# Optimization experiments

Measured on AMD Instinct MI355X. Metric: run time of the kernel, lower is better.

Reference implementation:

```python
import jax, jax.numpy as jnp
import numpy as np

N, DIM, E = 50000, 128, 600000


def setup_inputs() -> dict:
    key = jax.random.key(0)
    ks = jax.random.split(key, 10)
    scale = 1.0 / np.sqrt(DIM)
    return {
        "s": jax.random.normal(ks[0], (N, DIM), jnp.float32),
        "v": jax.random.normal(ks[1], (N, 3, DIM), jnp.float32),
        "edge_index": jax.random.randint(ks[2], (2, E), 0, N, jnp.int32),
        # linear_q: Linear(dim, dim); stored as [in, out] so y = x @ W + b
        "Wq": jax.random.normal(ks[3], (DIM, DIM), jnp.float32) * scale,
        "bq": jnp.zeros((DIM,), jnp.float32),
        # linear_kv: Linear(dim, 3*dim)
        "Wkv": jax.random.normal(ks[4], (DIM, 3 * DIM), jnp.float32) * scale,
        "bkv": jnp.zeros((3 * DIM,), jnp.float32),
        # vec_mlp: Linear(dim, dim)
        "Wvec": jax.random.normal(ks[5], (DIM, DIM), jnp.float32) * scale,
        "bvec": jnp.zeros((DIM,), jnp.float32),
    }


def reference(s, v, edge_index, Wq, bq, Wkv, bkv, Wvec, bvec):
    n_nodes = s.shape[0]
    row, col = edge_index[0], edge_index[1]

    q = s @ Wq + bq                                   # [N, dim]
    kv = s @ Wkv + bkv                                # [N, 3*dim]
    k, v_s, v_v = jnp.split(kv, 3, axis=-1)           # each [N, dim]

    # edge attention weight: per-edge dot product of gathered q/k
    w = jnp.sum(q[row] * k[col], axis=-1, keepdims=True)   # [E, 1]

    edge_msg_s = w * v_s[col]                               # [E, dim]
    # [E,1,1] * [E,1,dim] * [E,3,dim] -> [E,3,dim]
    edge_msg_v = w[:, :, None] * v_v[col][:, None, :] * v[col]

    agg_s = jax.ops.segment_sum(edge_msg_s, row, num_segments=n_nodes)  # [N, dim]
    agg_v = jax.ops.segment_sum(edge_msg_v, row, num_segments=n_nodes)  # [N, 3, dim]

    s_out = s + agg_s
    v_out = v + (agg_v @ Wvec + bvec)
    return (s_out, v_out)
```

## Files before the change

### kernel.cpp

```cpp
#include <hip/hip_runtime.h>
#include <hip/hip_bf16.h>

typedef __attribute__((ext_vector_type(8))) __bf16 bf16x8;
typedef __attribute__((ext_vector_type(4))) float f32x4;


__global__ void hist_kernel(const int* __restrict__ row, int* __restrict__ cnt, int e) {
  int i = blockIdx.x * 256 + threadIdx.x;
  if (i < e) atomicAdd(&cnt[row[i]], 1);
}

__global__ __launch_bounds__(1024) void scan1_kernel(const int* __restrict__ cnt, int* __restrict__ off,
                                                     int* __restrict__ bsum, int n) {
  __shared__ int sh[1024];
  int tid = threadIdx.x;
  int i = blockIdx.x * 1024 + tid;
  int v = (i < n) ? cnt[i] : 0;
  sh[tid] = v;
  __syncthreads();
  for (int d = 1; d < 1024; d <<= 1) {
    int t = (tid >= d) ? sh[tid - d] : 0;
    __syncthreads();
    sh[tid] += t;
    __syncthreads();
  }
  if (i < n) off[i] = sh[tid] - v;
  if (tid == 1023) bsum[blockIdx.x] = sh[1023];
}

__global__ void scan2_kernel(int* bsum, int nb) {
  if (blockIdx.x == 0 && threadIdx.x == 0) {
    int run = 0;
    for (int b = 0; b < nb; b++) { int t = bsum[b]; bsum[b] = run; run += t; }
  }
}

__global__ __launch_bounds__(1024) void scan3_kernel(const int* __restrict__ bsum, int* __restrict__ off,
                                                     int* __restrict__ cursor, int n, int e) {
  int i = blockIdx.x * 1024 + threadIdx.x;
  if (i < n) { int o = off[i] + bsum[blockIdx.x]; off[i] = o; cursor[i] = o; }
  if (i == 0) off[n] = e;
}

__global__ void scatter_kernel(const int* __restrict__ row, const int* __restrict__ col,
                               int* __restrict__ cursor, int* __restrict__ scol, int e) {
  int i = blockIdx.x * 256 + threadIdx.x;
  if (i < e) { int r = row[i]; int pos = atomicAdd(&cursor[r], 1); scol[pos] = col[i]; }
}


__global__ void wprep_kernel(const float* __restrict__ Wq, const float* __restrict__ Wkv,
                             const float* __restrict__ Wvec, __bf16* __restrict__ Wt) {
  int idx = blockIdx.x * 256 + threadIdx.x;
  int c = idx >> 7, k = idx & 127;
  float w;
  if (c < 128)      w = Wq[k * 128 + c];
  else if (c < 512) w = Wkv[k * 384 + (c - 128)];
  else              w = Wvec[k * 128 + (c - 512)];
  Wt[idx] = (__bf16)w;
}


__global__ __launch_bounds__(256) void gemm1_mfma(
    const float* __restrict__ s, const __bf16* __restrict__ Wtg,
    const float* __restrict__ bq, const float* __restrict__ bkv,
    const float* __restrict__ v,
    __bf16* __restrict__ qb, __bf16* __restrict__ nodebuf, int n)
{
  __shared__ __bf16 sA[64 * 136];
  __shared__ char uB[34816];
  __bf16* sB = (__bf16*)uB;
  float*  sO = (float*)uB;

  const int tid = threadIdx.x;
  const int y = blockIdx.y;
  const int n0 = blockIdx.x * 64;
  const int drow = tid >> 2, dseg = tid & 3;
  const int dgn = n0 + drow;

  {
    float4 f[8];
    if (dgn < n) {
      #pragma unroll
      for (int i = 0; i < 8; i++)
        f[i] = *(const float4*)&s[(size_t)dgn * 128 + dseg * 32 + i * 4];
    } else {
      #pragma unroll
      for (int i = 0; i < 8; i++) f[i] = make_float4(0.f, 0.f, 0.f, 0.f);
    }
    #pragma unroll
    for (int i = 0; i < 4; i++) {
      bf16x8 pk;
      pk[0] = (__bf16)f[2*i].x;   pk[1] = (__bf16)f[2*i].y;
      pk[2] = (__bf16)f[2*i].z;   pk[3] = (__bf16)f[2*i].w;
      pk[4] = (__bf16)f[2*i+1].x; pk[5] = (__bf16)f[2*i+1].y;
      pk[6] = (__bf16)f[2*i+1].z; pk[7] = (__bf16)f[2*i+1].w;
      *(bf16x8*)&sA[drow * 136 + dseg * 32 + i * 8] = pk;
    }
  }
  {
    int row = tid >> 1, half = tid & 1;
    const __bf16* src = &Wtg[(size_t)(y * 128 + row) * 128 + half * 64];
    #pragma unroll
    for (int i = 0; i < 8; i++)
      *(bf16x8*)&sB[row * 136 + half * 64 + i * 8] = *(const bf16x8*)&src[i * 8];
  }
  __syncthreads();

  const int wave = tid >> 6, lane = tid & 63;
  const int lr = lane & 15, lg = lane >> 4;

  bf16x8 a[4];
  #pragma unroll
  for (int ks = 0; ks < 4; ks++)
    a[ks] = *(const bf16x8*)&sA[(wave * 16 + lr) * 136 + ks * 32 + lg * 8];

  f32x4 acc[8];
  #pragma unroll
  for (int cf = 0; cf < 8; cf++) {
    f32x4 c = {0.f, 0.f, 0.f, 0.f};
    #pragma unroll
    for (int ks = 0; ks < 4; ks++) {
      bf16x8 b = *(const bf16x8*)&sB[(cf * 16 + lr) * 136 + ks * 32 + lg * 8];
      c = __builtin_amdgcn_mfma_f32_16x16x32_bf16(a[ks], b, c, 0, 0, 0);
    }
    acc[cf] = c;
  }
  __syncthreads();

  #pragma unroll
  for (int cf = 0; cf < 8; cf++) {
    int cl = cf * 16 + lr;
    #pragma unroll
    for (int r = 0; r < 4; r++)
      sO[(wave * 16 + lg * 4 + r) * 132 + cl] = acc[cf][r];
  }
  __syncthreads();

  if (dgn < n) {
    if (y == 0) {
      #pragma unroll
      for (int i = 0; i < 4; i++) {
        int c0 = dseg * 32 + i * 8;
        bf16x8 pk;
        #pragma unroll
        for (int j = 0; j < 8; j++)
          pk[j] = (__bf16)(sO[drow * 132 + c0 + j] + bq[c0 + j]);
        *(bf16x8*)&qb[(size_t)dgn * 128 + c0] = pk;
      }
    } else if (y == 1 || y == 2) {
      const int boff = (y - 1) * 128;
      #pragma unroll
      for (int i = 0; i < 4; i++) {
        int c0 = dseg * 32 + i * 8;
        bf16x8 pk;
        #pragma unroll
        for (int j = 0; j < 8; j++)
          pk[j] = (__bf16)(sO[drow * 132 + c0 + j] + bkv[boff + c0 + j]);
        *(bf16x8*)&nodebuf[(size_t)dgn * 640 + boff + c0] = pk;
      }
    } else {
      float vv[32];
      #pragma unroll
      for (int j = 0; j < 32; j++)
        vv[j] = sO[drow * 132 + dseg * 32 + j] + bkv[256 + dseg * 32 + j];
      #pragma unroll
      for (int j3 = 0; j3 < 3; j3++) {
        #pragma unroll
        for (int i = 0; i < 4; i++) {
          int c0 = dseg * 32 + i * 8;
          float4 va = *(const float4*)&v[((size_t)dgn * 3 + j3) * 128 + c0];
          float4 vb = *(const float4*)&v[((size_t)dgn * 3 + j3) * 128 + c0 + 4];
          bf16x8 pk;
          pk[0] = (__bf16)(vv[i*8+0] * va.x); pk[1] = (__bf16)(vv[i*8+1] * va.y);
          pk[2] = (__bf16)(vv[i*8+2] * va.z); pk[3] = (__bf16)(vv[i*8+3] * va.w);
          pk[4] = (__bf16)(vv[i*8+4] * vb.x); pk[5] = (__bf16)(vv[i*8+5] * vb.y);
          pk[6] = (__bf16)(vv[i*8+6] * vb.z); pk[7] = (__bf16)(vv[i*8+7] * vb.w);
          *(bf16x8*)&nodebuf[(size_t)dgn * 640 + 256 + j3 * 128 + c0] = pk;
        }
      }
    }
  }
}


__device__ inline float2 bf2f(unsigned u) {
  float2 r;
  r.x = __uint_as_float((u & 0xffffu) << 16);
  r.y = __uint_as_float(u & 0xffff0000u);
  return r;
}

__device__ __forceinline__ float dpp_add(float x, const int ctrl) {
  int t;
  switch (ctrl) {
    case 0:  t = __builtin_amdgcn_update_dpp(0, __float_as_int(x), 0xB1, 0xF, 0xF, true); break;
    case 1:  t = __builtin_amdgcn_update_dpp(0, __float_as_int(x), 0x4E, 0xF, 0xF, true); break;
    case 2:  t = __builtin_amdgcn_update_dpp(0, __float_as_int(x), 0x141, 0xF, 0xF, true); break;
    default: t = __builtin_amdgcn_update_dpp(0, __float_as_int(x), 0x140, 0xF, 0xF, true); break;
  }
  return x + __int_as_float(t);
}

__device__ __forceinline__ float row16_sum(float x) {
  x = dpp_add(x, 0);
  x = dpp_add(x, 1);
  x = dpp_add(x, 2);
  x = dpp_add(x, 3);
  return x;
}

#define ACCP(arr, vec) do { float2 _t;                                                \
  _t = bf2f(vec.x); arr[0].x = fmaf(d, _t.x, arr[0].x); arr[0].y = fmaf(d, _t.y, arr[0].y); \
  _t = bf2f(vec.y); arr[1].x = fmaf(d, _t.x, arr[1].x); arr[1].y = fmaf(d, _t.y, arr[1].y); \
  _t = bf2f(vec.z); arr[2].x = fmaf(d, _t.x, arr[2].x); arr[2].y = fmaf(d, _t.y, arr[2].y); \
  _t = bf2f(vec.w); arr[3].x = fmaf(d, _t.x, arr[3].x); arr[3].y = fmaf(d, _t.y, arr[3].y); \
} while (0)

template<bool B16>
__global__ __launch_bounds__(256) void agg_kernel(
    const int* __restrict__ off, const int* __restrict__ scol,
    const __bf16* __restrict__ qb, const char* __restrict__ nodebuf,
    const float* __restrict__ s, float* __restrict__ s_out,
    float* __restrict__ aggvf, __bf16* __restrict__ aggv16, int n)
{
  const int wid = threadIdx.x >> 6;
  const int lane = threadIdx.x & 63;
  const int nid = blockIdx.x * 4 + wid;
  if (nid >= n) return;
  const int slot = lane >> 4;
  const int fl = lane & 15;

  float qf[8];
  {
    uint4 qu = *(const uint4*)&qb[(size_t)nid * 128 + fl * 8];
    float2 t;
    t = bf2f(qu.x); qf[0] = t.x; qf[1] = t.y;
    t = bf2f(qu.y); qf[2] = t.x; qf[3] = t.y;
    t = bf2f(qu.z); qf[4] = t.x; qf[5] = t.y;
    t = bf2f(qu.w); qf[6] = t.x; qf[7] = t.y;
  }

  float2 acs[4], a0[4], a1[4], a2[4];
  #pragma unroll
  for (int i = 0; i < 4; i++) {
    acs[i] = make_float2(0.f, 0.f); a0[i] = make_float2(0.f, 0.f);
    a1[i] = make_float2(0.f, 0.f); a2[i] = make_float2(0.f, 0.f);
  }

  const int beg = off[nid];
  const int deg = off[nid + 1] - beg;

  for (int chunk = 0; chunk < deg; chunk += 64) {
    const int cc = (deg - chunk < 64) ? (deg - chunk) : 64;
    int myc = (lane < cc) ? scol[beg + chunk + lane] : 0;

    int c0 = __shfl(myc, (slot < cc) ? slot : 0);
    const char* g = nodebuf + (size_t)c0 * 1280 + fl * 16;
    uint4 ku = *(const uint4*)(g);
    uint4 vs = *(const uint4*)(g + 256);
    uint4 p0 = *(const uint4*)(g + 512);
    uint4 p1 = *(const uint4*)(g + 768);
    uint4 p2 = *(const uint4*)(g + 1024);

    for (int j = 0; j < cc; j += 4) {
      const bool more = (j + 4 < cc);
      uint4 nku, nvs, np0, np1, np2;
      if (more) {
        int ni = j + 4 + slot;
        int cn = __shfl(myc, (ni < cc) ? ni : 0);
        const char* gn = nodebuf + (size_t)cn * 1280 + fl * 16;
        nku = *(const uint4*)(gn);
        nvs = *(const uint4*)(gn + 256);
        np0 = *(const uint4*)(gn + 512);
        np1 = *(const uint4*)(gn + 768);
        np2 = *(const uint4*)(gn + 1024);
      }

      float2 t;
      float d = 0.f;
      t = bf2f(ku.x); d = fmaf(qf[0], t.x, d); d = fmaf(qf[1], t.y, d);
      t = bf2f(ku.y); d = fmaf(qf[2], t.x, d); d = fmaf(qf[3], t.y, d);
      t = bf2f(ku.z); d = fmaf(qf[4], t.x, d); d = fmaf(qf[5], t.y, d);
      t = bf2f(ku.w); d = fmaf(qf[6], t.x, d); d = fmaf(qf[7], t.y, d);
      d = row16_sum(d);
      if (j + slot >= cc) d = 0.f;

      ACCP(acs, vs); ACCP(a0, p0); ACCP(a1, p1); ACCP(a2, p2);

      if (more) { ku = nku; vs = nvs; p0 = np0; p1 = np1; p2 = np2; }
    }
  }

  #pragma unroll
  for (int i = 0; i < 4; i++) {
    acs[i].x += __shfl_xor(acs[i].x, 16); acs[i].x += __shfl_xor(acs[i].x, 32);
    acs[i].y += __shfl_xor(acs[i].y, 16); acs[i].y += __shfl_xor(acs[i].y, 32);
    a0[i].x  += __shfl_xor(a0[i].x, 16);  a0[i].x  += __shfl_xor(a0[i].x, 32);
    a0[i].y  += __shfl_xor(a0[i].y, 16);  a0[i].y  += __shfl_xor(a0[i].y, 32);
    a1[i].x  += __shfl_xor(a1[i].x, 16);  a1[i].x  += __shfl_xor(a1[i].x, 32);
    a1[i].y  += __shfl_xor(a1[i].y, 16);  a1[i].y  += __shfl_xor(a1[i].y, 32);
    a2[i].x  += __shfl_xor(a2[i].x, 16);  a2[i].x  += __shfl_xor(a2[i].x, 32);
    a2[i].y  += __shfl_xor(a2[i].y, 16);  a2[i].y  += __shfl_xor(a2[i].y, 32);
  }

  if (slot == 0) {
    const float* sp = &s[(size_t)nid * 128 + fl * 8];
    float4 w0, w1;
    w0.x = acs[0].x + sp[0]; w0.y = acs[0].y + sp[1];
    w0.z = acs[1].x + sp[2]; w0.w = acs[1].y + sp[3];
    w1.x = acs[2].x + sp[4]; w1.y = acs[2].y + sp[5];
    w1.z = acs[3].x + sp[6]; w1.w = acs[3].y + sp[7];
    *(float4*)&s_out[(size_t)nid * 128 + fl * 8] = w0;
    *(float4*)&s_out[(size_t)nid * 128 + fl * 8 + 4] = w1;

    if (B16) {
      bf16x8 pk;
      pk[0] = (__bf16)a0[0].x; pk[1] = (__bf16)a0[0].y; pk[2] = (__bf16)a0[1].x; pk[3] = (__bf16)a0[1].y;
      pk[4] = (__bf16)a0[2].x; pk[5] = (__bf16)a0[2].y; pk[6] = (__bf16)a0[3].x; pk[7] = (__bf16)a0[3].y;
      *(bf16x8*)&aggv16[((size_t)nid * 3 + 0) * 128 + fl * 8] = pk;
      pk[0] = (__bf16)a1[0].x; pk[1] = (__bf16)a1[0].y; pk[2] = (__bf16)a1[1].x; pk[3] = (__bf16)a1[1].y;
      pk[4] = (__bf16)a1[2].x; pk[5] = (__bf16)a1[2].y; pk[6] = (__bf16)a1[3].x; pk[7] = (__bf16)a1[3].y;
      *(bf16x8*)&aggv16[((size_t)nid * 3 + 1) * 128 + fl * 8] = pk;
      pk[0] = (__bf16)a2[0].x; pk[1] = (__bf16)a2[0].y; pk[2] = (__bf16)a2[1].x; pk[3] = (__bf16)a2[1].y;
      pk[4] = (__bf16)a2[2].x; pk[5] = (__bf16)a2[2].y; pk[6] = (__bf16)a2[3].x; pk[7] = (__bf16)a2[3].y;
      *(bf16x8*)&aggv16[((size_t)nid * 3 + 2) * 128 + fl * 8] = pk;
    } else {
      float* av = &aggvf[(size_t)nid * 384 + fl * 8];
      *(float4*)&av[0]   = make_float4(a0[0].x, a0[0].y, a0[1].x, a0[1].y);
      *(float4*)&av[4]   = make_float4(a0[2].x, a0[2].y, a0[3].x, a0[3].y);
      *(float4*)&av[128] = make_float4(a1[0].x, a1[0].y, a1[1].x, a1[1].y);
      *(float4*)&av[132] = make_float4(a1[2].x, a1[2].y, a1[3].x, a1[3].y);
      *(float4*)&av[256] = make_float4(a2[0].x, a2[0].y, a2[1].x, a2[1].y);
      *(float4*)&av[260] = make_float4(a2[2].x, a2[2].y, a2[3].x, a2[3].y);
    }
  }
}


template<bool B16>
__global__ __launch_bounds__(256) void gemm2_mfma(
    const __bf16* __restrict__ Wtg,
    const float* __restrict__ bvec, const float* __restrict__ v,
    const __bf16* __restrict__ aggv16, float* __restrict__ vout, int rows)
{
  __shared__ __bf16 sA[64 * 136];
  __shared__ char uB[34816];
  __bf16* sB = (__bf16*)uB;
  float*  sO = (float*)uB;

  const int tid = threadIdx.x;
  const int r0 = blockIdx.x * 64;
  const int drow = tid >> 2, dseg = tid & 3;
  const int dgr = r0 + drow;

  if (B16) {
    #pragma unroll
    for (int i = 0; i < 4; i++) {
      bf16x8 pk = {0,0,0,0,0,0,0,0};
      if (dgr < rows) pk = *(const bf16x8*)&aggv16[(size_t)dgr * 128 + dseg * 32 + i * 8];
      *(bf16x8*)&sA[drow * 136 + dseg * 32 + i * 8] = pk;
    }
  } else {
    float4 f[8];
    if (dgr < rows) {
      #pragma unroll
      for (int i = 0; i < 8; i++)
        f[i] = *(const float4*)&vout[(size_t)dgr * 128 + dseg * 32 + i * 4];
    } else {
      #pragma unroll
      for (int i = 0; i < 8; i++) f[i] = make_float4(0.f, 0.f, 0.f, 0.f);
    }
    #pragma unroll
    for (int i = 0; i < 4; i++) {
      bf16x8 pk;
      pk[0] = (__bf16)f[2*i].x;   pk[1] = (__bf16)f[2*i].y;
      pk[2] = (__bf16)f[2*i].z;   pk[3] = (__bf16)f[2*i].w;
      pk[4] = (__bf16)f[2*i+1].x; pk[5] = (__bf16)f[2*i+1].y;
      pk[6] = (__bf16)f[2*i+1].z; pk[7] = (__bf16)f[2*i+1].w;
      *(bf16x8*)&sA[drow * 136 + dseg * 32 + i * 8] = pk;
    }
  }
  {
    int row = tid >> 1, half = tid & 1;
    const __bf16* src = &Wtg[(size_t)(512 + row) * 128 + half * 64];
    #pragma unroll
    for (int i = 0; i < 8; i++)
      *(bf16x8*)&sB[row * 136 + half * 64 + i * 8] = *(const bf16x8*)&src[i * 8];
  }
  __syncthreads();

  const int wave = tid >> 6, lane = tid & 63;
  const int lr = lane & 15, lg = lane >> 4;

  bf16x8 a[4];
  #pragma unroll
  for (int ks = 0; ks < 4; ks++)
    a[ks] = *(const bf16x8*)&sA[(wave * 16 + lr) * 136 + ks * 32 + lg * 8];

  f32x4 acc[8];
  #pragma unroll
  for (int cf = 0; cf < 8; cf++) {
    f32x4 c = {0.f, 0.f, 0.f, 0.f};
    #pragma unroll
    for (int ks = 0; ks < 4; ks++) {
      bf16x8 b = *(const bf16x8*)&sB[(cf * 16 + lr) * 136 + ks * 32 + lg * 8];
      c = __builtin_amdgcn_mfma_f32_16x16x32_bf16(a[ks], b, c, 0, 0, 0);
    }
    acc[cf] = c;
  }
  __syncthreads();

  #pragma unroll
  for (int cf = 0; cf < 8; cf++) {
    int cl = cf * 16 + lr;
    #pragma unroll
    for (int r = 0; r < 4; r++)
      sO[(wave * 16 + lg * 4 + r) * 132 + cl] = acc[cf][r];
  }
  __syncthreads();

  if (dgr < rows) {
    #pragma unroll
    for (int i = 0; i < 8; i++) {
      int c0 = dseg * 32 + i * 4;
      float4 va = *(const float4*)&v[(size_t)dgr * 128 + c0];
      float4 o;
      o.x = sO[drow * 132 + c0 + 0] + va.x + bvec[c0 + 0];
      o.y = sO[drow * 132 + c0 + 1] + va.y + bvec[c0 + 1];
      o.z = sO[drow * 132 + c0 + 2] + va.z + bvec[c0 + 2];
      o.w = sO[drow * 132 + c0 + 3] + va.w + bvec[c0 + 3];
      *(float4*)&vout[(size_t)dgr * 128 + c0] = o;
    }
  }
}


extern "C" void kernel_launch(void* const* d_in, const int* in_sizes, int n_in,
                              void* d_out, int out_size, void* d_ws, size_t ws_size,
                              hipStream_t stream)
{
  const float* s    = (const float*)d_in[0];
  const float* v    = (const float*)d_in[1];
  const int*   ei   = (const int*)d_in[2];
  const float* Wq   = (const float*)d_in[3];
  const float* bq   = (const float*)d_in[4];
  const float* Wkv  = (const float*)d_in[5];
  const float* bkv  = (const float*)d_in[6];
  const float* Wvec = (const float*)d_in[7];
  const float* bvec = (const float*)d_in[8];

  const int N = in_sizes[0] / 128;
  const int E = in_sizes[2] / 2;
  const int* row = ei;
  const int* col = ei + E;

  char* ws = (char*)d_ws;
  size_t o = 0;
  auto alloc = [&](size_t bytes) -> char* {
    char* p = ws + o;
    o = (o + bytes + 255) & ~(size_t)255;
    return p;
  };
  int* off    = (int*)alloc((size_t)(N + 1) * 4);
  int* cursor = (int*)alloc((size_t)N * 4);
  int* bsum   = (int*)alloc(4096);
  int* scol   = (int*)alloc((size_t)E * 4);
  __bf16* qb      = (__bf16*)alloc((size_t)N * 128 * 2);
  __bf16* nodebuf = (__bf16*)alloc((size_t)N * 640 * 2);
  __bf16* Wt      = (__bf16*)alloc((size_t)640 * 128 * 2);
  __bf16* aggv16  = (__bf16*)alloc((size_t)N * 384 * 2);
  const bool b16 = (o <= ws_size);

  float* s_out = (float*)d_out;
  float* aggv  = (float*)d_out + (size_t)N * 128;

  hipMemsetAsync(cursor, 0, (size_t)N * 4, stream);
  hist_kernel<<<(E + 255) / 256, 256, 0, stream>>>(row, cursor, E);
  int nb = (N + 1023) / 1024;
  scan1_kernel<<<nb, 1024, 0, stream>>>(cursor, off, bsum, N);
  scan2_kernel<<<1, 64, 0, stream>>>(bsum, nb);
  scan3_kernel<<<nb, 1024, 0, stream>>>(bsum, off, cursor, N, E);
  scatter_kernel<<<(E + 255) / 256, 256, 0, stream>>>(row, col, cursor, scol, E);

  wprep_kernel<<<320, 256, 0, stream>>>(Wq, Wkv, Wvec, Wt);
  dim3 g1((N + 63) / 64, 4);
  gemm1_mfma<<<g1, 256, 0, stream>>>(s, Wt, bq, bkv, v, qb, nodebuf, N);

  if (b16)
    agg_kernel<true><<<(N + 3) / 4, 256, 0, stream>>>(off, scol, qb, (const char*)nodebuf,
                                                      s, s_out, aggv, aggv16, N);
  else
    agg_kernel<false><<<(N + 3) / 4, 256, 0, stream>>>(off, scol, qb, (const char*)nodebuf,
                                                       s, s_out, aggv, aggv16, N);

  if (b16)
    gemm2_mfma<true><<<(3 * N + 63) / 64, 256, 0, stream>>>(Wt, bvec, v, aggv16, aggv, 3 * N);
  else
    gemm2_mfma<false><<<(3 * N + 63) / 64, 256, 0, stream>>>(Wt, bvec, v, aggv16, aggv, 3 * N);
}
```

Measured before the change: 321.2 us.

## Fuse setup kernels and double-buffer edge gathers in aggregation

Merges the weight-transpose kernel into the histogram kernel and drops the single-thread block-sum scan by having each scan3 block reduce its preceding block sums itself, which removes two kernel launches. The aggregation loop now keeps two register sets of gathered neighbor data in flight, alternating between them, so the next group's loads overlap the current group's math. This raises register pressure in the aggregation kernel, and out-of-range slots now load the last valid neighbor instead of neighbor 0.

```diff
diff --git a/kernel.cpp b/kernel.cpp
--- a/kernel.cpp
+++ b/kernel.cpp
@@ -5,9 +5,24 @@
 typedef __attribute__((ext_vector_type(4))) float f32x4;
 
 
-__global__ void hist_kernel(const int* __restrict__ row, int* __restrict__ cnt, int e) {
-  int i = blockIdx.x * 256 + threadIdx.x;
-  if (i < e) atomicAdd(&cnt[row[i]], 1);
+__global__ void hist_wprep_kernel(const int* __restrict__ row, int* __restrict__ cnt, int e,
+                                  const float* __restrict__ Wq, const float* __restrict__ Wkv,
+                                  const float* __restrict__ Wvec, __bf16* __restrict__ Wt,
+                                  int nbh) {
+  if ((int)blockIdx.x < nbh) {
+    int i = blockIdx.x * 256 + threadIdx.x;
+    if (i < e) atomicAdd(&cnt[row[i]], 1);
+  } else {
+    int idx = (blockIdx.x - nbh) * 256 + threadIdx.x;
+    if (idx < 81920) {
+      int c = idx >> 7, k = idx & 127;
+      float w;
+      if (c < 128)      w = Wq[k * 128 + c];
+      else if (c < 512) w = Wkv[k * 384 + (c - 128)];
+      else              w = Wvec[k * 128 + (c - 512)];
+      Wt[idx] = (__bf16)w;
+    }
+  }
 }
 
 __global__ __launch_bounds__(1024) void scan1_kernel(const int* __restrict__ cnt, int* __restrict__ off,
@@ -28,17 +43,21 @@
   if (tid == 1023) bsum[blockIdx.x] = sh[1023];
 }
 
-__global__ void scan2_kernel(int* bsum, int nb) {
-  if (blockIdx.x == 0 && threadIdx.x == 0) {
-    int run = 0;
-    for (int b = 0; b < nb; b++) { int t = bsum[b]; bsum[b] = run; run += t; }
-  }
-}
-
 __global__ __launch_bounds__(1024) void scan3_kernel(const int* __restrict__ bsum, int* __restrict__ off,
                                                      int* __restrict__ cursor, int n, int e) {
-  int i = blockIdx.x * 1024 + threadIdx.x;
-  if (i < n) { int o = off[i] + bsum[blockIdx.x]; off[i] = o; cursor[i] = o; }
+  __shared__ int base_sh;
+  const int tid = threadIdx.x;
+  if (tid < 64) {
+    int part = 0;
+    for (int b = tid; b < (int)blockIdx.x; b += 64) part += bsum[b];
+    #pragma unroll
+    for (int m = 32; m >= 1; m >>= 1) part += __shfl_xor(part, m);
+    if (tid == 0) base_sh = part;
+  }
+  __syncthreads();
+  const int base = base_sh;
+  int i = blockIdx.x * 1024 + tid;
+  if (i < n) { int o = off[i] + base; off[i] = o; cursor[i] = o; }
   if (i == 0) off[n] = e;
 }
 
@@ -46,18 +65,6 @@
                                int* __restrict__ cursor, int* __restrict__ scol, int e) {
   int i = blockIdx.x * 256 + threadIdx.x;
   if (i < e) { int r = row[i]; int pos = atomicAdd(&cursor[r], 1); scol[pos] = col[i]; }
-}
-
-
-__global__ void wprep_kernel(const float* __restrict__ Wq, const float* __restrict__ Wkv,
-                             const float* __restrict__ Wvec, __bf16* __restrict__ Wt) {
-  int idx = blockIdx.x * 256 + threadIdx.x;
-  int c = idx >> 7, k = idx & 127;
-  float w;
-  if (c < 128)      w = Wq[k * 128 + c];
-  else if (c < 512) w = Wkv[k * 384 + (c - 128)];
-  else              w = Wvec[k * 128 + (c - 512)];
-  Wt[idx] = (__bf16)w;
 }
 
 
@@ -210,6 +217,20 @@
   return x;
 }
 
+struct EdgeRegs { uint4 ku, vs, p0, p1, p2; };
+
+__device__ __forceinline__ void issue_group(const char* __restrict__ nodebuf, int myc,
+                                            int g, int cc, int slot, int fl, EdgeRegs& R) {
+  int ei = g * 4 + slot;
+  int c = __shfl(myc, (ei < cc) ? ei : (cc - 1));
+  const char* gp = nodebuf + (size_t)c * 1280 + fl * 16;
+  R.ku = *(const uint4*)(gp);
+  R.vs = *(const uint4*)(gp + 256);
+  R.p0 = *(const uint4*)(gp + 512);
+  R.p1 = *(const uint4*)(gp + 768);
+  R.p2 = *(const uint4*)(gp + 1024);
+}
+
 #define ACCP(arr, vec) do { float2 _t;                                                \
   _t = bf2f(vec.x); arr[0].x = fmaf(d, _t.x, arr[0].x); arr[0].y = fmaf(d, _t.y, arr[0].y); \
   _t = bf2f(vec.y); arr[1].x = fmaf(d, _t.x, arr[1].x); arr[1].y = fmaf(d, _t.y, arr[1].y); \
@@ -254,42 +275,32 @@
   for (int chunk = 0; chunk < deg; chunk += 64) {
     const int cc = (deg - chunk < 64) ? (deg - chunk) : 64;
     int myc = (lane < cc) ? scol[beg + chunk + lane] : 0;
-
-    int c0 = __shfl(myc, (slot < cc) ? slot : 0);
-    const char* g = nodebuf + (size_t)c0 * 1280 + fl * 16;
-    uint4 ku = *(const uint4*)(g);
-    uint4 vs = *(const uint4*)(g + 256);
-    uint4 p0 = *(const uint4*)(g + 512);
-    uint4 p1 = *(const uint4*)(g + 768);
-    uint4 p2 = *(const uint4*)(g + 1024);
-
-    for (int j = 0; j < cc; j += 4) {
-      const bool more = (j + 4 < cc);
-      uint4 nku, nvs, np0, np1, np2;
-      if (more) {
-        int ni = j + 4 + slot;
-        int cn = __shfl(myc, (ni < cc) ? ni : 0);
-        const char* gn = nodebuf + (size_t)cn * 1280 + fl * 16;
-        nku = *(const uint4*)(gn);
-        nvs = *(const uint4*)(gn + 256);
-        np0 = *(const uint4*)(gn + 512);
-        np1 = *(const uint4*)(gn + 768);
-        np2 = *(const uint4*)(gn + 1024);
-      }
-
-      float2 t;
-      float d = 0.f;
-      t = bf2f(ku.x); d = fmaf(qf[0], t.x, d); d = fmaf(qf[1], t.y, d);
-      t = bf2f(ku.y); d = fmaf(qf[2], t.x, d); d = fmaf(qf[3], t.y, d);
-      t = bf2f(ku.z); d = fmaf(qf[4], t.x, d); d = fmaf(qf[5], t.y, d);
-      t = bf2f(ku.w); d = fmaf(qf[6], t.x, d); d = fmaf(qf[7], t.y, d);
-      d = row16_sum(d);
-      if (j + slot >= cc) d = 0.f;
-
-      ACCP(acs, vs); ACCP(a0, p0); ACCP(a1, p1); ACCP(a2, p2);
-
-      if (more) { ku = nku; vs = nvs; p0 = np0; p1 = np1; p2 = np2; }
-    }
+    const int ng = (cc + 3) >> 2;
+
+    EdgeRegs A, B;
+    issue_group(nodebuf, myc, 0, cc, slot, fl, A);
+    if (ng > 1) issue_group(nodebuf, myc, 1, cc, slot, fl, B);
+
+    #define COMPUTE(gidx, R) do {                                                  \
+      float2 t; float d = 0.f;                                                     \
+      t = bf2f(R.ku.x); d = fmaf(qf[0], t.x, d); d = fmaf(qf[1], t.y, d);          \
+      t = bf2f(R.ku.y); d = fmaf(qf[2], t.x, d); d = fmaf(qf[3], t.y, d);          \
+      t = bf2f(R.ku.z); d = fmaf(qf[4], t.x, d); d = fmaf(qf[5], t.y, d);          \
+      t = bf2f(R.ku.w); d = fmaf(qf[6], t.x, d); d = fmaf(qf[7], t.y, d);          \
+      d = row16_sum(d);                                                            \
+      if ((gidx) * 4 + slot >= cc) d = 0.f;                                        \
+      ACCP(acs, R.vs); ACCP(a0, R.p0); ACCP(a1, R.p1); ACCP(a2, R.p2);             \
+    } while (0)
+
+    int g = 0;
+    for (; g + 1 < ng; g += 2) {
+      COMPUTE(g, A);
+      if (g + 2 < ng) issue_group(nodebuf, myc, g + 2, cc, slot, fl, A);
+      COMPUTE(g + 1, B);
+      if (g + 3 < ng) issue_group(nodebuf, myc, g + 3, cc, slot, fl, B);
+    }
+    if (g < ng) COMPUTE(g, A);
+    #undef COMPUTE
   }
 
   #pragma unroll
@@ -476,14 +487,13 @@
   float* aggv  = (float*)d_out + (size_t)N * 128;
 
   hipMemsetAsync(cursor, 0, (size_t)N * 4, stream);
-  hist_kernel<<<(E + 255) / 256, 256, 0, stream>>>(row, cursor, E);
+  int nbh = (E + 255) / 256;
+  hist_wprep_kernel<<<nbh + 320, 256, 0, stream>>>(row, cursor, E, Wq, Wkv, Wvec, Wt, nbh);
   int nb = (N + 1023) / 1024;
   scan1_kernel<<<nb, 1024, 0, stream>>>(cursor, off, bsum, N);
-  scan2_kernel<<<1, 64, 0, stream>>>(bsum, nb);
   scan3_kernel<<<nb, 1024, 0, stream>>>(bsum, off, cursor, N, E);
   scatter_kernel<<<(E + 255) / 256, 256, 0, stream>>>(row, col, cursor, scol, E);
 
-  wprep_kernel<<<320, 256, 0, stream>>>(Wq, Wkv, Wvec, Wt);
   dim3 g1((N + 63) / 64, 4);
   gemm1_mfma<<<g1, 256, 0, stream>>>(s, Wt, bq, bkv, v, qb, nodebuf, N);
 
```

Measured after the change: 311.0 us. 3.2% less time.

## Fold Wq·Wk into one matrix and gather raw s instead of k and v_s

Applied to the files above, without the earlier changes.

Rewrites the attention score q·k as s_row·(Wq Wk^T)·s_col plus bias terms. Per-edge gathers now read raw bf16 s_col instead of separate k and v_s rows, which shrinks the node buffer from 640 to 512 bf16 per node. The scalar aggregate g = sum w·s_col then goes through a post-aggregation GEMM with Wvs, fused into one launch with the Wvec GEMM. It also merges the histogram and weight-prep kernels and drops the serial scan2 kernel, adding extra bf16 rounding of the folded weights and g.

```diff
diff --git a/kernel.cpp b/kernel.cpp
--- a/kernel.cpp
+++ b/kernel.cpp
@@ -5,9 +5,52 @@
 typedef __attribute__((ext_vector_type(4))) float f32x4;
 
 
-__global__ void hist_kernel(const int* __restrict__ row, int* __restrict__ cnt, int e) {
-  int i = blockIdx.x * 256 + threadIdx.x;
-  if (i < e) atomicAdd(&cnt[row[i]], 1);
+__global__ void prep_kernel(const int* __restrict__ row, int* __restrict__ cnt, int e,
+                            const float* __restrict__ Wq, const float* __restrict__ Wkv,
+                            const float* __restrict__ Wvec, const float* __restrict__ bq,
+                            __bf16* __restrict__ Wt, float* __restrict__ bM,
+                            float* __restrict__ m2, float* __restrict__ c0, int nbh) {
+  const int bid = blockIdx.x, tid = threadIdx.x;
+  if (bid < nbh) {
+    int i = bid * 256 + tid;
+    if (i < e) atomicAdd(&cnt[row[i]], 1);
+  } else if (bid < nbh + 256) {
+    int idx = (bid - nbh) * 256 + tid;
+    int c = 128 + (idx >> 7), k = idx & 127;
+    float w = (c < 512) ? Wkv[k * 384 + (c - 128)] : Wvec[k * 128 + (c - 512)];
+    Wt[c * 128 + k] = (__bf16)w;
+  } else if (bid < nbh + 256 + 128) {
+    __shared__ float wk[128];
+    int c = bid - (nbh + 256);
+    if (tid < 128) wk[tid] = Wkv[tid * 0 + c * 384 + tid];
+    __syncthreads();
+    if (tid < 128) {
+      float acc = 0.f;
+      #pragma unroll 8
+      for (int j = 0; j < 128; j++) acc += Wq[tid * 128 + j] * wk[j];
+      Wt[c * 128 + tid] = (__bf16)acc;
+    } else if (tid == 128) {
+      float acc = 0.f;
+      for (int j = 0; j < 128; j++) acc += bq[j] * wk[j];
+      bM[c] = acc;
+    }
+  } else {
+  }
+}
+
+__global__ void m2_kernel(const float* __restrict__ Wq, const float* __restrict__ bq,
+                          const float* __restrict__ bkv, float* __restrict__ m2,
+                          float* __restrict__ c0) {
+  int tid = threadIdx.x;
+  if (tid < 128) {
+    float acc = 0.f;
+    for (int j = 0; j < 128; j++) acc += Wq[tid * 128 + j] * bkv[j];
+    m2[tid] = acc;
+  } else if (tid == 128) {
+    float acc = 0.f;
+    for (int j = 0; j < 128; j++) acc += bq[j] * bkv[j];
+    c0[0] = acc;
+  }
 }
 
 __global__ __launch_bounds__(1024) void scan1_kernel(const int* __restrict__ cnt, int* __restrict__ off,
@@ -28,17 +71,21 @@
   if (tid == 1023) bsum[blockIdx.x] = sh[1023];
 }
 
-__global__ void scan2_kernel(int* bsum, int nb) {
-  if (blockIdx.x == 0 && threadIdx.x == 0) {
-    int run = 0;
-    for (int b = 0; b < nb; b++) { int t = bsum[b]; bsum[b] = run; run += t; }
-  }
-}
-
 __global__ __launch_bounds__(1024) void scan3_kernel(const int* __restrict__ bsum, int* __restrict__ off,
                                                      int* __restrict__ cursor, int n, int e) {
-  int i = blockIdx.x * 1024 + threadIdx.x;
-  if (i < n) { int o = off[i] + bsum[blockIdx.x]; off[i] = o; cursor[i] = o; }
+  __shared__ int base_sh;
+  const int tid = threadIdx.x;
+  if (tid < 64) {
+    int part = 0;
+    for (int b = tid; b < (int)blockIdx.x; b += 64) part += bsum[b];
+    #pragma unroll
+    for (int m = 32; m >= 1; m >>= 1) part += __shfl_xor(part, m);
+    if (tid == 0) base_sh = part;
+  }
+  __syncthreads();
+  const int base = base_sh;
+  int i = blockIdx.x * 1024 + tid;
+  if (i < n) { int o = off[i] + base; off[i] = o; cursor[i] = o; }
   if (i == 0) off[n] = e;
 }
 
@@ -49,26 +96,17 @@
 }
 
 
-__global__ void wprep_kernel(const float* __restrict__ Wq, const float* __restrict__ Wkv,
-                             const float* __restrict__ Wvec, __bf16* __restrict__ Wt) {
-  int idx = blockIdx.x * 256 + threadIdx.x;
-  int c = idx >> 7, k = idx & 127;
-  float w;
-  if (c < 128)      w = Wq[k * 128 + c];
-  else if (c < 512) w = Wkv[k * 384 + (c - 128)];
-  else              w = Wvec[k * 128 + (c - 512)];
-  Wt[idx] = (__bf16)w;
-}
-
-
 __global__ __launch_bounds__(256) void gemm1_mfma(
     const float* __restrict__ s, const __bf16* __restrict__ Wtg,
-    const float* __restrict__ bq, const float* __restrict__ bkv,
+    const float* __restrict__ bM, const float* __restrict__ bkv,
+    const float* __restrict__ m2, const float* __restrict__ c0,
     const float* __restrict__ v,
-    __bf16* __restrict__ qb, __bf16* __restrict__ nodebuf, int n)
+    __bf16* __restrict__ qb, float* __restrict__ beta,
+    __bf16* __restrict__ nodebuf, int n)
 {
   __shared__ __bf16 sA[64 * 136];
   __shared__ char uB[34816];
+  __shared__ float sBeta[64][4];
   __bf16* sB = (__bf16*)uB;
   float*  sO = (float*)uB;
 
@@ -100,7 +138,8 @@
   }
   {
     int row = tid >> 1, half = tid & 1;
-    const __bf16* src = &Wtg[(size_t)(y * 128 + row) * 128 + half * 64];
+    int brow = (y == 0) ? row : 384 + row;
+    const __bf16* src = &Wtg[(size_t)brow * 128 + half * 64];
     #pragma unroll
     for (int i = 0; i < 8; i++)
       *(bf16x8*)&sB[row * 136 + half * 64 + i * 8] = *(const bf16x8*)&src[i * 8];
@@ -137,47 +176,49 @@
   }
   __syncthreads();
 
-  if (dgn < n) {
-    if (y == 0) {
+  if (y == 0) {
+    float part = 0.f;
+    #pragma unroll 8
+    for (int j = 0; j < 32; j++)
+      part += (float)sA[drow * 136 + dseg * 32 + j] * m2[dseg * 32 + j];
+    sBeta[drow][dseg] = part;
+    __syncthreads();
+    if (dgn < n) {
+      if (dseg == 0)
+        beta[dgn] = sBeta[drow][0] + sBeta[drow][1] + sBeta[drow][2] + sBeta[drow][3] + c0[0];
       #pragma unroll
       for (int i = 0; i < 4; i++) {
-        int c0 = dseg * 32 + i * 8;
+        int cc = dseg * 32 + i * 8;
         bf16x8 pk;
         #pragma unroll
         for (int j = 0; j < 8; j++)
-          pk[j] = (__bf16)(sO[drow * 132 + c0 + j] + bq[c0 + j]);
-        *(bf16x8*)&qb[(size_t)dgn * 128 + c0] = pk;
+          pk[j] = (__bf16)(sO[drow * 132 + cc + j] + bM[cc + j]);
+        *(bf16x8*)&qb[(size_t)dgn * 128 + cc] = pk;
       }
-    } else if (y == 1 || y == 2) {
-      const int boff = (y - 1) * 128;
+    }
+  } else if (dgn < n) {
+    #pragma unroll
+    for (int i = 0; i < 4; i++) {
+      int cc = dseg * 32 + i * 8;
+      *(bf16x8*)&nodebuf[(size_t)dgn * 512 + cc] = *(const bf16x8*)&sA[drow * 136 + cc];
+    }
+    float vv[32];
+    #pragma unroll
+    for (int j = 0; j < 32; j++)
+      vv[j] = sO[drow * 132 + dseg * 32 + j] + bkv[256 + dseg * 32 + j];
+    #pragma unroll
+    for (int j3 = 0; j3 < 3; j3++) {
       #pragma unroll
       for (int i = 0; i < 4; i++) {
-        int c0 = dseg * 32 + i * 8;
+        int cc = dseg * 32 + i * 8;
+        float4 va = *(const float4*)&v[((size_t)dgn * 3 + j3) * 128 + cc];
+        float4 vb = *(const float4*)&v[((size_t)dgn * 3 + j3) * 128 + cc + 4];
         bf16x8 pk;
-        #pragma unroll
-        for (int j = 0; j < 8; j++)
-          pk[j] = (__bf16)(sO[drow * 132 + c0 + j] + bkv[boff + c0 + j]);
-        *(bf16x8*)&nodebuf[(size_t)dgn * 640 + boff + c0] = pk;
-      }
-    } else {
-      float vv[32];
-      #pragma unroll
-      for (int j = 0; j < 32; j++)
-        vv[j] = sO[drow * 132 + dseg * 32 + j] + bkv[256 + dseg * 32 + j];
-      #pragma unroll
-      for (int j3 = 0; j3 < 3; j3++) {
-        #pragma unroll
-        for (int i = 0; i < 4; i++) {
-          int c0 = dseg * 32 + i * 8;
-          float4 va = *(const float4*)&v[((size_t)dgn * 3 + j3) * 128 + c0];
-          float4 vb = *(const float4*)&v[((size_t)dgn * 3 + j3) * 128 + c0 + 4];
-          bf16x8 pk;
-          pk[0] = (__bf16)(vv[i*8+0] * va.x); pk[1] = (__bf16)(vv[i*8+1] * va.y);
-          pk[2] = (__bf16)(vv[i*8+2] * va.z); pk[3] = (__bf16)(vv[i*8+3] * va.w);
-          pk[4] = (__bf16)(vv[i*8+4] * vb.x); pk[5] = (__bf16)(vv[i*8+5] * vb.y);
-          pk[6] = (__bf16)(vv[i*8+6] * vb.z); pk[7] = (__bf16)(vv[i*8+7] * vb.w);
-          *(bf16x8*)&nodebuf[(size_t)dgn * 640 + 256 + j3 * 128 + c0] = pk;
-        }
+        pk[0] = (__bf16)(vv[i*8+0] * va.x); pk[1] = (__bf16)(vv[i*8+1] * va.y);
+        pk[2] = (__bf16)(vv[i*8+2] * va.z); pk[3] = (__bf16)(vv[i*8+3] * va.w);
+        pk[4] = (__bf16)(vv[i*8+4] * vb.x); pk[5] = (__bf16)(vv[i*8+5] * vb.y);
+        pk[6] = (__bf16)(vv[i*8+6] * vb.z); pk[7] = (__bf16)(vv[i*8+7] * vb.w);
+        *(bf16x8*)&nodebuf[(size_t)dgn * 512 + 128 + j3 * 128 + cc] = pk;
       }
     }
   }
@@ -203,10 +244,7 @@
 }
 
 __device__ __forceinline__ float row16_sum(float x) {
-  x = dpp_add(x, 0);
-  x = dpp_add(x, 1);
-  x = dpp_add(x, 2);
-  x = dpp_add(x, 3);
+  x = dpp_add(x, 0); x = dpp_add(x, 1); x = dpp_add(x, 2); x = dpp_add(x, 3);
   return x;
 }
 
@@ -217,12 +255,12 @@
   _t = bf2f(vec.w); arr[3].x = fmaf(d, _t.x, arr[3].x); arr[3].y = fmaf(d, _t.y, arr[3].y); \
 } while (0)
 
-template<bool B16>
 __global__ __launch_bounds__(256) void agg_kernel(
     const int* __restrict__ off, const int* __restrict__ scol,
-    const __bf16* __restrict__ qb, const char* __restrict__ nodebuf,
-    const float* __restrict__ s, float* __restrict__ s_out,
-    float* __restrict__ aggvf, __bf16* __restrict__ aggv16, int n)
+    const __bf16* __restrict__ qb, const float* __restrict__ beta,
+    const char* __restrict__ nodebuf,
+    __bf16* __restrict__ gb, float* __restrict__ W1,
+    __bf16* __restrict__ aggv16, int n)
 {
   const int wid = threadIdx.x >> 6;
   const int lane = threadIdx.x & 63;
@@ -240,11 +278,13 @@
     t = bf2f(qu.z); qf[4] = t.x; qf[5] = t.y;
     t = bf2f(qu.w); qf[6] = t.x; qf[7] = t.y;
   }
-
-  float2 acs[4], a0[4], a1[4], a2[4];
+  const float betar = beta[nid];
+
+  float2 g[4], a0[4], a1[4], a2[4];
+  float ws = 0.f;
   #pragma unroll
   for (int i = 0; i < 4; i++) {
-    acs[i] = make_float2(0.f, 0.f); a0[i] = make_float2(0.f, 0.f);
+    g[i] = make_float2(0.f, 0.f); a0[i] = make_float2(0.f, 0.f);
     a1[i] = make_float2(0.f, 0.f); a2[i] = make_float2(0.f, 0.f);
   }
 
@@ -255,94 +295,85 @@
     const int cc = (deg - chunk < 64) ? (deg - chunk) : 64;
     int myc = (lane < cc) ? scol[beg + chunk + lane] : 0;
 
-    int c0 = __shfl(myc, (slot < cc) ? slot : 0);
-    const char* g = nodebuf + (size_t)c0 * 1280 + fl * 16;
-    uint4 ku = *(const uint4*)(g);
-    uint4 vs = *(const uint4*)(g + 256);
-    uint4 p0 = *(const uint4*)(g + 512);
-    uint4 p1 = *(const uint4*)(g + 768);
-    uint4 p2 = *(const uint4*)(g + 1024);
+    int c0i = __shfl(myc, (slot < cc) ? slot : 0);
+    const char* gp = nodebuf + (size_t)c0i * 1024 + fl * 16;
+    uint4 sc = *(const uint4*)(gp);
+    uint4 p0 = *(const uint4*)(gp + 256);
+    uint4 p1 = *(const uint4*)(gp + 512);
+    uint4 p2 = *(const uint4*)(gp + 768);
 
     for (int j = 0; j < cc; j += 4) {
       const bool more = (j + 4 < cc);
-      uint4 nku, nvs, np0, np1, np2;
+      uint4 nsc, np0, np1, np2;
       if (more) {
         int ni = j + 4 + slot;
         int cn = __shfl(myc, (ni < cc) ? ni : 0);
-        const char* gn = nodebuf + (size_t)cn * 1280 + fl * 16;
-        nku = *(const uint4*)(gn);
-        nvs = *(const uint4*)(gn + 256);
-        np0 = *(const uint4*)(gn + 512);
-        np1 = *(const uint4*)(gn + 768);
-        np2 = *(const uint4*)(gn + 1024);
+        const char* gn = nodebuf + (size_t)cn * 1024 + fl * 16;
+        nsc = *(const uint4*)(gn);
+        np0 = *(const uint4*)(gn + 256);
+        np1 = *(const uint4*)(gn + 512);
+        np2 = *(const uint4*)(gn + 768);
       }
 
-      float2 t;
+      float2 t0 = bf2f(sc.x), t1 = bf2f(sc.y), t2 = bf2f(sc.z), t3 = bf2f(sc.w);
       float d = 0.f;
-      t = bf2f(ku.x); d = fmaf(qf[0], t.x, d); d = fmaf(qf[1], t.y, d);
-      t = bf2f(ku.y); d = fmaf(qf[2], t.x, d); d = fmaf(qf[3], t.y, d);
-      t = bf2f(ku.z); d = fmaf(qf[4], t.x, d); d = fmaf(qf[5], t.y, d);
-      t = bf2f(ku.w); d = fmaf(qf[6], t.x, d); d = fmaf(qf[7], t.y, d);
-      d = row16_sum(d);
+      d = fmaf(qf[0], t0.x, d); d = fmaf(qf[1], t0.y, d);
+      d = fmaf(qf[2], t1.x, d); d = fmaf(qf[3], t1.y, d);
+      d = fmaf(qf[4], t2.x, d); d = fmaf(qf[5], t2.y, d);
+      d = fmaf(qf[6], t3.x, d); d = fmaf(qf[7], t3.y, d);
+      d = row16_sum(d) + betar;
       if (j + slot >= cc) d = 0.f;
 
-      ACCP(acs, vs); ACCP(a0, p0); ACCP(a1, p1); ACCP(a2, p2);
-
-      if (more) { ku = nku; vs = nvs; p0 = np0; p1 = np1; p2 = np2; }
-    }
-  }
-
+      g[0].x = fmaf(d, t0.x, g[0].x); g[0].y = fmaf(d, t0.y, g[0].y);
+      g[1].x = fmaf(d, t1.x, g[1].x); g[1].y = fmaf(d, t1.y, g[1].y);
+      g[2].x = fmaf(d, t2.x, g[2].x); g[2].y = fmaf(d, t2.y, g[2].y);
+      g[3].x = fmaf(d, t3.x, g[3].x); g[3].y = fmaf(d, t3.y, g[3].y);
+      ws += d;
+      ACCP(a0, p0); ACCP(a1, p1); ACCP(a2, p2);
+
+      if (more) { sc = nsc; p0 = np0; p1 = np1; p2 = np2; }
+    }
+  }
+
+  ws += __shfl_xor(ws, 16); ws += __shfl_xor(ws, 32);
   #pragma unroll
   for (int i = 0; i < 4; i++) {
-    acs[i].x += __shfl_xor(acs[i].x, 16); acs[i].x += __shfl_xor(acs[i].x, 32);
-    acs[i].y += __shfl_xor(acs[i].y, 16); acs[i].y += __shfl_xor(acs[i].y, 32);
-    a0[i].x  += __shfl_xor(a0[i].x, 16);  a0[i].x  += __shfl_xor(a0[i].x, 32);
-    a0[i].y  += __shfl_xor(a0[i].y, 16);  a0[i].y  += __shfl_xor(a0[i].y, 32);
-    a1[i].x  += __shfl_xor(a1[i].x, 16);  a1[i].x  += __shfl_xor(a1[i].x, 32);
-    a1[i].y  += __shfl_xor(a1[i].y, 16);  a1[i].y  += __shfl_xor(a1[i].y, 32);
-    a2[i].x  += __shfl_xor(a2[i].x, 16);  a2[i].x  += __shfl_xor(a2[i].x, 32);
-    a2[i].y  += __shfl_xor(a2[i].y, 16);  a2[i].y  += __shfl_xor(a2[i].y, 32);
+    g[i].x  += __shfl_xor(g[i].x, 16);  g[i].x  += __shfl_xor(g[i].x, 32);
+    g[i].y  += __shfl_xor(g[i].y, 16);  g[i].y  += __shfl_xor(g[i].y, 32);
+    a0[i].x += __shfl_xor(a0[i].x, 16); a0[i].x += __shfl_xor(a0[i].x, 32);
+    a0[i].y += __shfl_xor(a0[i].y, 16); a0[i].y += __shfl_xor(a0[i].y, 32);
+    a1[i].x += __shfl_xor(a1[i].x, 16); a1[i].x += __shfl_xor(a1[i].x, 32);
+    a1[i].y += __shfl_xor(a1[i].y, 16); a1[i].y += __shfl_xor(a1[i].y, 32);
+    a2[i].x += __shfl_xor(a2[i].x, 16); a2[i].x += __shfl_xor(a2[i].x, 32);
+    a2[i].y += __shfl_xor(a2[i].y, 16); a2[i].y += __shfl_xor(a2[i].y, 32);
   }
 
   if (slot == 0) {
-    const float* sp = &s[(size_t)nid * 128 + fl * 8];
-    float4 w0, w1;
-    w0.x = acs[0].x + sp[0]; w0.y = acs[0].y + sp[1];
-    w0.z = acs[1].x + sp[2]; w0.w = acs[1].y + sp[3];
-    w1.x = acs[2].x + sp[4]; w1.y = acs[2].y + sp[5];
-    w1.z = acs[3].x + sp[6]; w1.w = acs[3].y + sp[7];
-    *(float4*)&s_out[(size_t)nid * 128 + fl * 8] = w0;
-    *(float4*)&s_out[(size_t)nid * 128 + fl * 8 + 4] = w1;
-
-    if (B16) {
-      bf16x8 pk;
-      pk[0] = (__bf16)a0[0].x; pk[1] = (__bf16)a0[0].y; pk[2] = (__bf16)a0[1].x; pk[3] = (__bf16)a0[1].y;
-      pk[4] = (__bf16)a0[2].x; pk[5] = (__bf16)a0[2].y; pk[6] = (__bf16)a0[3].x; pk[7] = (__bf16)a0[3].y;
-      *(bf16x8*)&aggv16[((size_t)nid * 3 + 0) * 128 + fl * 8] = pk;
-      pk[0] = (__bf16)a1[0].x; pk[1] = (__bf16)a1[0].y; pk[2] = (__bf16)a1[1].x; pk[3] = (__bf16)a1[1].y;
-      pk[4] = (__bf16)a1[2].x; pk[5] = (__bf16)a1[2].y; pk[6] = (__bf16)a1[3].x; pk[7] = (__bf16)a1[3].y;
-      *(bf16x8*)&aggv16[((size_t)nid * 3 + 1) * 128 + fl * 8] = pk;
-      pk[0] = (__bf16)a2[0].x; pk[1] = (__bf16)a2[0].y; pk[2] = (__bf16)a2[1].x; pk[3] = (__bf16)a2[1].y;
-      pk[4] = (__bf16)a2[2].x; pk[5] = (__bf16)a2[2].y; pk[6] = (__bf16)a2[3].x; pk[7] = (__bf16)a2[3].y;
-      *(bf16x8*)&aggv16[((size_t)nid * 3 + 2) * 128 + fl * 8] = pk;
-    } else {
-      float* av = &aggvf[(size_t)nid * 384 + fl * 8];
-      *(float4*)&av[0]   = make_float4(a0[0].x, a0[0].y, a0[1].x, a0[1].y);
-      *(float4*)&av[4]   = make_float4(a0[2].x, a0[2].y, a0[3].x, a0[3].y);
-      *(float4*)&av[128] = make_float4(a1[0].x, a1[0].y, a1[1].x, a1[1].y);
-      *(float4*)&av[132] = make_float4(a1[2].x, a1[2].y, a1[3].x, a1[3].y);
-      *(float4*)&av[256] = make_float4(a2[0].x, a2[0].y, a2[1].x, a2[1].y);
-      *(float4*)&av[260] = make_float4(a2[2].x, a2[2].y, a2[3].x, a2[3].y);
-    }
-  }
-}
-
-
-template<bool B16>
-__global__ __launch_bounds__(256) void gemm2_mfma(
-    const __bf16* __restrict__ Wtg,
-    const float* __restrict__ bvec, const float* __restrict__ v,
-    const __bf16* __restrict__ aggv16, float* __restrict__ vout, int rows)
+    bf16x8 pk;
+    pk[0] = (__bf16)g[0].x; pk[1] = (__bf16)g[0].y; pk[2] = (__bf16)g[1].x; pk[3] = (__bf16)g[1].y;
+    pk[4] = (__bf16)g[2].x; pk[5] = (__bf16)g[2].y; pk[6] = (__bf16)g[3].x; pk[7] = (__bf16)g[3].y;
+    *(bf16x8*)&gb[(size_t)nid * 128 + fl * 8] = pk;
+    if (fl == 0) W1[nid] = ws;
+
+    pk[0] = (__bf16)a0[0].x; pk[1] = (__bf16)a0[0].y; pk[2] = (__bf16)a0[1].x; pk[3] = (__bf16)a0[1].y;
+    pk[4] = (__bf16)a0[2].x; pk[5] = (__bf16)a0[2].y; pk[6] = (__bf16)a0[3].x; pk[7] = (__bf16)a0[3].y;
+    *(bf16x8*)&aggv16[((size_t)nid * 3 + 0) * 128 + fl * 8] = pk;
+    pk[0] = (__bf16)a1[0].x; pk[1] = (__bf16)a1[0].y; pk[2] = (__bf16)a1[1].x; pk[3] = (__bf16)a1[1].y;
+    pk[4] = (__bf16)a1[2].x; pk[5] = (__bf16)a1[2].y; pk[6] = (__bf16)a1[3].x; pk[7] = (__bf16)a1[3].y;
+    *(bf16x8*)&aggv16[((size_t)nid * 3 + 1) * 128 + fl * 8] = pk;
+    pk[0] = (__bf16)a2[0].x; pk[1] = (__bf16)a2[0].y; pk[2] = (__bf16)a2[1].x; pk[3] = (__bf16)a2[1].y;
+    pk[4] = (__bf16)a2[2].x; pk[5] = (__bf16)a2[2].y; pk[6] = (__bf16)a2[3].x; pk[7] = (__bf16)a2[3].y;
+    *(bf16x8*)&aggv16[((size_t)nid * 3 + 2) * 128 + fl * 8] = pk;
+  }
+}
+
+
+__global__ __launch_bounds__(256) void gemm23_mfma(
+    const __bf16* __restrict__ Wtg, const float* __restrict__ bkv, const float* __restrict__ bvec,
+    const float* __restrict__ s, const float* __restrict__ v,
+    const __bf16* __restrict__ gb, const float* __restrict__ W1,
+    const __bf16* __restrict__ aggv16,
+    float* __restrict__ s_out, float* __restrict__ vout, int n, int nb1)
 {
   __shared__ __bf16 sA[64 * 136];
   __shared__ char uB[34816];
@@ -350,40 +381,25 @@
   float*  sO = (float*)uB;
 
   const int tid = threadIdx.x;
-  const int r0 = blockIdx.x * 64;
+  const bool smode = (int)blockIdx.x < nb1;
+  const int r0 = smode ? blockIdx.x * 64 : (blockIdx.x - nb1) * 64;
+  const int rows = smode ? n : 3 * n;
   const int drow = tid >> 2, dseg = tid & 3;
   const int dgr = r0 + drow;
 
-  if (B16) {
+  {
+    const __bf16* Asrc = smode ? gb : aggv16;
     #pragma unroll
     for (int i = 0; i < 4; i++) {
       bf16x8 pk = {0,0,0,0,0,0,0,0};
-      if (dgr < rows) pk = *(const bf16x8*)&aggv16[(size_t)dgr * 128 + dseg * 32 + i * 8];
-      *(bf16x8*)&sA[drow * 136 + dseg * 32 + i * 8] = pk;
-    }
-  } else {
-    float4 f[8];
-    if (dgr < rows) {
-      #pragma unroll
-      for (int i = 0; i < 8; i++)
-        f[i] = *(const float4*)&vout[(size_t)dgr * 128 + dseg * 32 + i * 4];
-    } else {
-      #pragma unroll
-      for (int i = 0; i < 8; i++) f[i] = make_float4(0.f, 0.f, 0.f, 0.f);
-    }
-    #pragma unroll
-    for (int i = 0; i < 4; i++) {
-      bf16x8 pk;
-      pk[0] = (__bf16)f[2*i].x;   pk[1] = (__bf16)f[2*i].y;
-      pk[2] = (__bf16)f[2*i].z;   pk[3] = (__bf16)f[2*i].w;
-      pk[4] = (__bf16)f[2*i+1].x; pk[5] = (__bf16)f[2*i+1].y;
-      pk[6] = (__bf16)f[2*i+1].z; pk[7] = (__bf16)f[2*i+1].w;
+      if (dgr < rows) pk = *(const bf16x8*)&Asrc[(size_t)dgr * 128 + dseg * 32 + i * 8];
       *(bf16x8*)&sA[drow * 136 + dseg * 32 + i * 8] = pk;
     }
   }
   {
     int row = tid >> 1, half = tid & 1;
-    const __bf16* src = &Wtg[(size_t)(512 + row) * 128 + half * 64];
+    int brow = (smode ? 256 : 512) + row;
+    const __bf16* src = &Wtg[(size_t)brow * 128 + half * 64];
     #pragma unroll
     for (int i = 0; i < 8; i++)
       *(bf16x8*)&sB[row * 136 + half * 64 + i * 8] = *(const bf16x8*)&src[i * 8];
@@ -421,16 +437,31 @@
   __syncthreads();
 
   if (dgr < rows) {
-    #pragma unroll
-    for (int i = 0; i < 8; i++) {
-      int c0 = dseg * 32 + i * 4;
-      float4 va = *(const float4*)&v[(size_t)dgr * 128 + c0];
-      float4 o;
-      o.x = sO[drow * 132 + c0 + 0] + va.x + bvec[c0 + 0];
-      o.y = sO[drow * 132 + c0 + 1] + va.y + bvec[c0 + 1];
-      o.z = sO[drow * 132 + c0 + 2] + va.z + bvec[c0 + 2];
-      o.w = sO[drow * 132 + c0 + 3] + va.w + bvec[c0 + 3];
-      *(float4*)&vout[(size_t)dgr * 128 + c0] = o;
+    if (smode) {
+      const float w1 = W1[dgr];
+      #pragma unroll
+      for (int i = 0; i < 8; i++) {
+        int cc = dseg * 32 + i * 4;
+        float4 sa = *(const float4*)&s[(size_t)dgr * 128 + cc];
+        float4 o;
+        o.x = sO[drow * 132 + cc + 0] + sa.x + w1 * bkv[128 + cc + 0];
+        o.y = sO[drow * 132 + cc + 1] + sa.y + w1 * bkv[128 + cc + 1];
+        o.z = sO[drow * 132 + cc + 2] + sa.z + w1 * bkv[128 + cc + 2];
+        o.w = sO[drow * 132 + cc + 3] + sa.w + w1 * bkv[128 + cc + 3];
+        *(float4*)&s_out[(size_t)dgr * 128 + cc] = o;
+      }
+    } else {
+      #pragma unroll
+      for (int i = 0; i < 8; i++) {
+        int cc = dseg * 32 + i * 4;
+        float4 va = *(const float4*)&v[(size_t)dgr * 128 + cc];
+        float4 o;
+        o.x = sO[drow * 132 + cc + 0] + va.x + bvec[cc + 0];
+        o.y = sO[drow * 132 + cc + 1] + va.y + bvec[cc + 1];
+        o.z = sO[drow * 132 + cc + 2] + va.z + bvec[cc + 2];
+        o.w = sO[drow * 132 + cc + 3] + va.w + bvec[cc + 3];
+        *(float4*)&vout[(size_t)dgr * 128 + cc] = o;
+      }
     }
   }
 }
@@ -467,35 +498,37 @@
   int* bsum   = (int*)alloc(4096);
   int* scol   = (int*)alloc((size_t)E * 4);
   __bf16* qb      = (__bf16*)alloc((size_t)N * 128 * 2);
-  __bf16* nodebuf = (__bf16*)alloc((size_t)N * 640 * 2);
+  float*  beta    = (float*)alloc((size_t)N * 4);
+  float*  W1      = (float*)alloc((size_t)N * 4);
+  __bf16* nodebuf = (__bf16*)alloc((size_t)N * 512 * 2);
   __bf16* Wt      = (__bf16*)alloc((size_t)640 * 128 * 2);
   __bf16* aggv16  = (__bf16*)alloc((size_t)N * 384 * 2);
-  const bool b16 = (o <= ws_size);
+  __bf16* gb      = (__bf16*)alloc((size_t)N * 128 * 2);
+  float*  bM      = (float*)alloc(512);
+  float*  m2      = (float*)alloc(512);
+  float*  c0      = (float*)alloc(256);
 
   float* s_out = (float*)d_out;
-  float* aggv  = (float*)d_out + (size_t)N * 128;
+  float* vout  = (float*)d_out + (size_t)N * 128;
 
   hipMemsetAsync(cursor, 0, (size_t)N * 4, stream);
-  hist_kernel<<<(E + 255) / 256, 256, 0, stream>>>(row, cursor, E);
+  int nbh = (E + 255) / 256;
+  prep_kernel<<<nbh + 256 + 128, 256, 0, stream>>>(row, cursor, E, Wq, Wkv, Wvec, bq,
+                                                   Wt, bM, m2, c0, nbh);
+  m2_kernel<<<1, 256, 0, stream>>>(Wq, bq, bkv, m2, c0);
   int nb = (N + 1023) / 1024;
   scan1_kernel<<<nb, 1024, 0, stream>>>(cursor, off, bsum, N);
-  scan2_kernel<<<1, 64, 0, stream>>>(bsum, nb);
   scan3_kernel<<<nb, 1024, 0, stream>>>(bsum, off, cursor, N, E);
   scatter_kernel<<<(E + 255) / 256, 256, 0, stream>>>(row, col, cursor, scol, E);
 
-  wprep_kernel<<<320, 256, 0, stream>>>(Wq, Wkv, Wvec, Wt);
-  dim3 g1((N + 63) / 64, 4);
-  gemm1_mfma<<<g1, 256, 0, stream>>>(s, Wt, bq, bkv, v, qb, nodebuf, N);
-
-  if (b16)
-    agg_kernel<true><<<(N + 3) / 4, 256, 0, stream>>>(off, scol, qb, (const char*)nodebuf,
-                                                      s, s_out, aggv, aggv16, N);
-  else
-    agg_kernel<false><<<(N + 3) / 4, 256, 0, stream>>>(off, scol, qb, (const char*)nodebuf,
-                                                       s, s_out, aggv, aggv16, N);
-
-  if (b16)
-    gemm2_mfma<true><<<(3 * N + 63) / 64, 256, 0, stream>>>(Wt, bvec, v, aggv16, aggv, 3 * N);
-  else
-    gemm2_mfma<false><<<(3 * N + 63) / 64, 256, 0, stream>>>(Wt, bvec, v, aggv16, aggv, 3 * N);
-}
+  dim3 g1((N + 63) / 64, 2);
+  gemm1_mfma<<<g1, 256, 0, stream>>>(s, Wt, bM, bkv, m2, c0, v, qb, beta, nodebuf, N);
+
+  agg_kernel<<<(N + 3) / 4, 256, 0, stream>>>(off, scol, qb, beta, (const char*)nodebuf,
+                                              gb, W1, aggv16, N);
+
+  int nb1 = (N + 63) / 64;
+  int nb2 = (3 * N + 63) / 64;
+  gemm23_mfma<<<nb1 + nb2, 256, 0, stream>>>(Wt, bkv, bvec, s, v, gb, W1, aggv16,
+                                             s_out, vout, N, nb1);
+}
```

Result: faster. 299.0 us (-6.9%).
